# Optimization experiments

Hardware: AMD Instinct MI355X
Metric: run time of the kernel (lower is better)

## Reference

```python
import jax, jax.numpy as jnp
import numpy as np
import math

N_NODES = 20000
N_EDGES = 640000
N_BASIS = 10
NUM_NEIGHBORS = 32.0


def _fctp_scalar_attr(x0, x1, attr, W0, W1):
    """FullyConnectedTensorProduct(irreps_in, '0e' attr) == per-irrep linear
    scaled by the scalar attribute, with e3nn fan-in normalization.
    x0: [N, mul0] scalars, x1: [N, mul1, 3] vectors, attr: [N, 1]."""
    a = attr[:, :1]
    y0 = (x0 * a) @ W0 / jnp.sqrt(jnp.asarray(W0.shape[0], x0.dtype))
    y1 = jnp.einsum('nui,uv->nvi', x1 * a[:, :, None], W1) / jnp.sqrt(jnp.asarray(W1.shape[0], x1.dtype))
    return y0, y1


def setup_inputs() -> dict:
    key = jax.random.key(0)
    ks = jax.random.split(key, 13)
    node_input = jax.random.normal(ks[0], (N_NODES, 80), jnp.float32)
    node_attr = jnp.ones((N_NODES, 1), jnp.float32)
    edge_attr = jax.random.normal(ks[1], (N_EDGES, 4), jnp.float32)
    edge_scalars = jax.random.uniform(ks[2], (N_EDGES, N_BASIS), jnp.float32)
    edge_index = jax.random.randint(ks[3], (2, N_EDGES), 0, N_NODES)
    # learned params
    W_sc0 = jax.random.normal(ks[4], (32, 32), jnp.float32)
    W_sc1 = jax.random.normal(ks[5], (16, 16), jnp.float32)
    W_l1_0 = jax.random.normal(ks[6], (32, 32), jnp.float32)
    W_l1_1 = jax.random.normal(ks[7], (16, 16), jnp.float32)
    W_fc0 = jax.random.normal(ks[8], (N_BASIS, 64), jnp.float32)
    W_fc1 = jax.random.normal(ks[9], (64, 96), jnp.float32)  # 96 = tp.weight_numel
    W_l2_0 = jax.random.normal(ks[10], (48, 32), jnp.float32)
    W_l2_1 = jax.random.normal(ks[11], (48, 16), jnp.float32)
    return dict(node_input=node_input, node_attr=node_attr, edge_attr=edge_attr,
                edge_scalars=edge_scalars, W_sc0=W_sc0, W_sc1=W_sc1,
                W_l1_0=W_l1_0, W_l1_1=W_l1_1, W_fc0=W_fc0, W_fc1=W_fc1,
                W_l2_0=W_l2_0, W_l2_1=W_l2_1, edge_index=edge_index)


def reference(node_input, node_attr, edge_attr, edge_scalars,
              W_sc0, W_sc1, W_l1_0, W_l1_1, W_fc0, W_fc1, W_l2_0, W_l2_1,
              edge_index):
    N = node_input.shape[0]
    x0 = node_input[:, :32]                     # 32x0e
    x1 = node_input[:, 32:].reshape(N, 16, 3)   # 16x1o

    # self-connection and pre-TP linear
    s0, s1 = _fctp_scalar_attr(x0, x1, node_attr, W_sc0, W_sc1)
    y0, y1 = _fctp_scalar_attr(x0, x1, node_attr, W_l1_0, W_l1_1)

    # radial MLP -> per-edge TP weights (e3nn FullyConnectedNet: no bias, fan-in norm, silu)
    h = jax.nn.silu(edge_scalars @ W_fc0 / jnp.sqrt(jnp.asarray(N_BASIS, jnp.float32)))
    w = h @ W_fc1 / jnp.sqrt(jnp.asarray(64.0, jnp.float32))  # [E, 96]
    w_a, w_b, w_c, w_d = w[:, :32], w[:, 32:64], w[:, 64:80], w[:, 80:96]

    src, dst = edge_index[0], edge_index[1]
    xs0 = y0[src]                               # [E, 32]
    xs1 = y1[src]                               # [E, 16, 3]
    e0 = edge_attr[:, :1]                       # [E, 1] 0e sh
    e1 = edge_attr[:, 1:4]                      # [E, 3] 1o sh

    # 'uvu' tensor product paths -> irreps_mid = 32x0e + 16x0e + 32x1o + 16x1o
    m_a = w_a * xs0 * e0                                    # 0e x 0e -> 0e  [E,32]
    m_b = (w_b * xs0)[:, :, None] * e1[:, None, :]          # 0e x 1o -> 1o  [E,32,3]
    m_c = w_c[:, :, None] * xs1 * e0[:, :, None]            # 1o x 0e -> 1o  [E,16,3]
    m_d = w_d * jnp.einsum('eui,ei->eu', xs1, e1) / jnp.sqrt(jnp.asarray(3.0, jnp.float32))  # 1o x 1o -> 0e [E,16]
    mid0 = jnp.concatenate([m_a, m_d], axis=1)              # [E, 48] scalars
    mid1 = jnp.concatenate([m_b, m_c], axis=1)              # [E, 48, 3] vectors

    # scatter-add into destination nodes, normalized by sqrt(num_neighbors)
    inv = 1.0 / jnp.sqrt(jnp.asarray(NUM_NEIGHBORS, jnp.float32))
    agg0 = jax.ops.segment_sum(mid0, dst, num_segments=N) * inv
    agg1 = jax.ops.segment_sum(mid1, dst, num_segments=N) * inv

    # lin2: FCTP(irreps_mid, '0e') -> irreps_out, attr == 1
    z0 = agg0 @ W_l2_0 / jnp.sqrt(jnp.asarray(48.0, jnp.float32))
    z1 = jnp.einsum('nui,uv->nvi', agg1, W_l2_1) / jnp.sqrt(jnp.asarray(48.0, jnp.float32))

    # skip mix: output_mask of sc is all ones here (all out irreps reachable)
    c_s = math.sin(math.pi / 8)
    c_x = math.cos(math.pi / 8)
    out0 = c_s * s0 + c_x * z0
    out1 = c_s * s1 + c_x * z1
    return jnp.concatenate([out0, out1.reshape(N, 48)], axis=1)
```

## Files before the change

kernel.cpp:

```cpp
#include <hip/hip_runtime.h>

#define N_NODES 20000
#define N_EDGES 640000
#define N_MT (N_EDGES/16)

typedef short short8 __attribute__((ext_vector_type(8)));
typedef float f32x4 __attribute__((ext_vector_type(4)));

__device__ __forceinline__ unsigned short f2bf(float x){
  unsigned int u = __builtin_bit_cast(unsigned int, x);
  u += 0x7fffu + ((u >> 16) & 1u);
  return (unsigned short)(u >> 16);
}

__device__ __forceinline__ void wave_lds_fence(){
  __asm__ volatile("s_waitcnt lgkmcnt(0)" ::: "memory");
}

__global__ void k_y(const float* __restrict__ ni, const float* __restrict__ na,
                    const float* __restrict__ Wl10, const float* __restrict__ Wl11,
                    float* __restrict__ y){
  int gid = blockIdx.x*256 + threadIdx.x;
  if (gid >= N_NODES*80) return;
  int n = gid / 80, k = gid - n*80;
  const float* row = ni + (size_t)n*80;
  float a = na[n];
  float acc = 0.f;
  if (k < 32){
    #pragma unroll
    for (int u=0; u<32; ++u) acc += row[u]*Wl10[u*32+k];
    y[gid] = acc * a * 0.17677669529663687f;
  } else {
    int kk = k-32, v = kk/3, i = kk - v*3;
    #pragma unroll
    for (int u=0; u<16; ++u) acc += row[32+u*3+i]*Wl11[u*16+v];
    y[gid] = acc * a * 0.25f;
  }
}

__global__ void k_hist(const int* __restrict__ ei, int* __restrict__ counts){
  int e = blockIdx.x*256 + threadIdx.x;
  if (e < N_EDGES) atomicAdd(&counts[ei[N_EDGES + e]], 1);
}

__global__ void k_alloc(const int* __restrict__ counts, int* __restrict__ ctr,
                        int* __restrict__ cursor){
  int n = blockIdx.x*256 + threadIdx.x;
  if (n < N_NODES) cursor[n] = atomicAdd(ctr, counts[n]);
}

__global__ void k_fill(const int* __restrict__ ei, int* __restrict__ cursor,
                       int* __restrict__ eids, int* __restrict__ srcs,
                       int* __restrict__ dsts){
  int e = blockIdx.x*256 + threadIdx.x;
  if (e < N_EDGES){
    int d = ei[N_EDGES + e];
    int pos = atomicAdd(&cursor[d], 1);
    eids[pos] = e;
    srcs[pos] = ei[e];
    dsts[pos] = d;
  }
}

__global__ __launch_bounds__(256, 3) void k_edge(
    const float* __restrict__ edge_attr, const float* __restrict__ edge_scalars,
    const float* __restrict__ Wfc0, const float* __restrict__ Wfc1,
    const int* __restrict__ eids, const int* __restrict__ srcs,
    const int* __restrict__ dsts,
    const float* __restrict__ y, float* __restrict__ agg){
  __shared__ float s_wfc0[640];
  __shared__ float s_w [4][16*97];
  __shared__ float s_y [4][16*80];
  __shared__ float s_es[4][16*16];
  __shared__ float s_ea[4][16*4];

  const int t = threadIdx.x;
  const int w = t >> 6, l = t & 63;
  const int r = l & 15, part = l >> 4;

  for (int i = t; i < 640; i += 256) s_wfc0[i] = Wfc0[i];

  short8 b0[6], b1[6];
  #pragma unroll
  for (int nt=0; nt<6; ++nt){
    #pragma unroll
    for (int j=0; j<8; ++j){
      b0[nt][j] = (short)f2bf(Wfc1[(     part*8+j)*96 + nt*16 + r]);
      b1[nt][j] = (short)f2bf(Wfc1[(32 + part*8+j)*96 + nt*16 + r]);
    }
  }
  __syncthreads();

  int o_c[3], yo[3], eai[3];
  bool dot0;
  {
    #pragma unroll
    for (int p=0; p<3; ++p){
      int c = p*64 + l;
      if (c < 32)      { o_c[p]=c;    yo[p]=c;        eai[p]=0; }
      else if (c < 48) { int u=c-32;  o_c[p]=80+u;    yo[p]=32+3*u; eai[p]=0; }
      else if (c < 144){ int idx=c-48;  int u=idx/3, fi=idx-u*3; o_c[p]=32+u; yo[p]=u;        eai[p]=1+fi; }
      else             { int idx=c-144; int u=idx/3, i =idx-u*3; o_c[p]=64+u; yo[p]=32+3*u+i; eai[p]=0; }
    }
    dot0 = (l >= 32) && (l < 48);
  }

  float* sw  = s_w[w];
  float* sy  = s_y[w];
  float* ses = s_es[w];
  float* sea = s_ea[w];

  const int gw = blockIdx.x*4 + w;
  const int nw = gridDim.x*4;
  const int m0 = (int)(((long long)gw     * N_MT) / nw);
  const int m1 = (int)(((long long)(gw+1) * N_MT) / nw);

  float acc0 = 0.f, acc1 = 0.f, acc2 = 0.f;
  int dcur = -1;

  for (int m = m0; m < m1; ++m){
    const int base = m*16;
    const int eid  = eids[base + r];
    const int srcv = srcs[base + r];
    const int dstv = dsts[base + r];

    {
      const float* esp = edge_scalars + (size_t)eid*10;
      if (part == 0)      *(float4*)(ses + r*16    ) = *(const float4*)(esp);
      else if (part == 1) *(float4*)(ses + r*16 + 4) = *(const float4*)(esp + 4);
      else if (part == 2) *(float2*)(ses + r*16 + 8) = *(const float2*)(esp + 8);
      else                *(float4*)(sea + r*4     ) = *(const float4*)(edge_attr + (size_t)eid*4);
      const float* yp = y + (size_t)srcv*80 + part*20;
      float* syp = sy + r*80 + part*20;
      #pragma unroll
      for (int q=0; q<5; ++q)
        *(float4*)(syp + q*4) = *(const float4*)(yp + q*4);
    }
    wave_lds_fence();

    float hv0[8], hv1[8];
    #pragma unroll
    for (int j=0; j<8; ++j){ hv0[j]=0.f; hv1[j]=0.f; }
    {
      const float* esr = ses + r*16;
      #pragma unroll
      for (int k=0; k<10; ++k){
        float ev = esr[k];
        const float* wr = s_wfc0 + k*64 + part*8;
        #pragma unroll
        for (int j=0; j<8; ++j){ hv0[j] += ev*wr[j]; hv1[j] += ev*wr[32+j]; }
      }
    }
    short8 a0, a1;
    #pragma unroll
    for (int j=0; j<8; ++j){
      float x0 = hv0[j]*0.31622776601683794f;
      float x1 = hv1[j]*0.31622776601683794f;
      a0[j] = (short)f2bf(x0/(1.f+__expf(-x0)));
      a1[j] = (short)f2bf(x1/(1.f+__expf(-x1)));
    }

    #pragma unroll
    for (int nt=0; nt<6; ++nt){
      f32x4 acc = {0.f,0.f,0.f,0.f};
      acc = __builtin_amdgcn_mfma_f32_16x16x32_bf16(a0, b0[nt], acc, 0,0,0);
      acc = __builtin_amdgcn_mfma_f32_16x16x32_bf16(a1, b1[nt], acc, 0,0,0);
      #pragma unroll
      for (int rr=0; rr<4; ++rr)
        sw[(part*4+rr)*97 + nt*16 + r] = acc[rr]*0.125f;
    }
    wave_lds_fence();

    for (int e=0; e<16; ++e){
      int de = __shfl(dstv, e);
      if (de != dcur){
        if (dcur >= 0){
          unsafeAtomicAdd(&agg[(size_t)dcur*192 +       l], acc0);
          unsafeAtomicAdd(&agg[(size_t)dcur*192 +  64 + l], acc1);
          unsafeAtomicAdd(&agg[(size_t)dcur*192 + 128 + l], acc2);
        }
        acc0 = acc1 = acc2 = 0.f;
        dcur = de;
      }
      const float* swe  = sw  + e*97;
      const float* sye  = sy  + e*80;
      const float* seae = sea + e*4;
      float m0v;
      if (dot0){
        m0v = swe[o_c[0]] * (sye[yo[0]]*seae[1] + sye[yo[0]+1]*seae[2] + sye[yo[0]+2]*seae[3])
              * 0.5773502691896258f;
      } else {
        m0v = swe[o_c[0]] * sye[yo[0]] * seae[eai[0]];
      }
      acc0 += m0v;
      acc1 += swe[o_c[1]] * sye[yo[1]] * seae[eai[1]];
      acc2 += swe[o_c[2]] * sye[yo[2]] * seae[eai[2]];
    }
    wave_lds_fence();
  }
  if (dcur >= 0){
    unsafeAtomicAdd(&agg[(size_t)dcur*192 +       l], acc0);
    unsafeAtomicAdd(&agg[(size_t)dcur*192 +  64 + l], acc1);
    unsafeAtomicAdd(&agg[(size_t)dcur*192 + 128 + l], acc2);
  }
}

__global__ void k_finish(const float* __restrict__ ni, const float* __restrict__ na,
    const float* __restrict__ Wsc0, const float* __restrict__ Wsc1,
    const float* __restrict__ Wl20, const float* __restrict__ Wl21,
    const float* __restrict__ agg, float* __restrict__ out){
  int gid = blockIdx.x*256 + threadIdx.x;
  if (gid >= N_NODES*80) return;
  int n = gid / 80, k = gid - n*80;
  const float* row = ni + (size_t)n*80;
  const float* ag  = agg + (size_t)n*192;
  float a = na[n];
  const float c_s = 0.3826834323650898f;
  const float c_x = 0.9238795325112867f;
  const float zscale = 0.17677669529663687f * 0.14433756729740643f;
  float s = 0.f, z = 0.f;
  if (k < 32){
    #pragma unroll
    for (int u=0; u<32; ++u) s += row[u]*Wsc0[u*32+k];
    s *= a * 0.17677669529663687f;
    #pragma unroll
    for (int u=0; u<48; ++u) z += ag[u]*Wl20[u*32+k];
  } else {
    int kk=k-32, v=kk/3, i=kk-v*3;
    #pragma unroll
    for (int u=0; u<16; ++u) s += row[32+u*3+i]*Wsc1[u*16+v];
    s *= a * 0.25f;
    #pragma unroll
    for (int u=0; u<48; ++u) z += ag[48+u*3+i]*Wl21[u*16+v];
  }
  out[gid] = c_s*s + c_x*z*zscale;
}

extern "C" void kernel_launch(void* const* d_in, const int* in_sizes, int n_in,
                              void* d_out, int out_size, void* d_ws, size_t ws_size,
                              hipStream_t stream){
  const float* node_input   = (const float*)d_in[0];
  const float* node_attr    = (const float*)d_in[1];
  const float* edge_attr    = (const float*)d_in[2];
  const float* edge_scalars = (const float*)d_in[3];
  const float* W_sc0 = (const float*)d_in[4];
  const float* W_sc1 = (const float*)d_in[5];
  const float* W_l1_0 = (const float*)d_in[6];
  const float* W_l1_1 = (const float*)d_in[7];
  const float* W_fc0 = (const float*)d_in[8];
  const float* W_fc1 = (const float*)d_in[9];
  const float* W_l2_0 = (const float*)d_in[10];
  const float* W_l2_1 = (const float*)d_in[11];
  const int* edge_index = (const int*)d_in[12];
  float* out = (float*)d_out;

  char* ws = (char*)d_ws;
  float* y    = (float*)ws;
  float* agg  = (float*)(ws + 6400000);
  int* counts = (int*)(ws + 6400000 + 15360000);
  int* ctr    = counts + 20000;
  int* cursor = counts + 20008;
  int* eids   = cursor + 20000;
  int* srcs   = eids + N_EDGES;
  int* dsts   = srcs + N_EDGES;

  hipMemsetAsync(agg, 0, (size_t)N_NODES*192*sizeof(float), stream);
  hipMemsetAsync(counts, 0, (size_t)(20008)*sizeof(int), stream);

  k_hist <<<(N_EDGES+255)/256, 256, 0, stream>>>(edge_index, counts);
  k_alloc<<<(N_NODES+255)/256, 256, 0, stream>>>(counts, ctr, cursor);
  k_fill <<<(N_EDGES+255)/256, 256, 0, stream>>>(edge_index, cursor, eids, srcs, dsts);
  k_y    <<<(N_NODES*80+255)/256, 256, 0, stream>>>(node_input, node_attr, W_l1_0, W_l1_1, y);
  k_edge <<<768, 256, 0, stream>>>(edge_attr, edge_scalars, W_fc0, W_fc1,
                                   eids, srcs, dsts, y, agg);
  k_finish<<<(N_NODES*80+255)/256, 256, 0, stream>>>(node_input, node_attr, W_sc0, W_sc1,
                                                     W_l2_0, W_l2_1, agg, out);
}
```

Before: 381.7 us.

## Pack sorted edge metadata, prefetch next tile, fuse histogram with node linear

The fill kernel now writes a packed 64-byte record per sorted edge holding src, dst, edge_attr and edge_scalars, so the edge kernel reads one contiguous, coalesced float4 per lane instead of gathering through eids. The edge kernel software-pipelines the work: the next tile's metadata and source-node y rows are loaded into registers while the current tile's MLP and MFMA run. Edge scalars now reach lanes by shuffles rather than LDS, and the LDS row stride for the weights changes. The histogram and y kernels are merged into one launch. The cost is an extra 41MB scattered write in k_fill and higher register pressure from the prefetch buffers.

Measured after the change: 579.3 us. +51.8%, slower.

```diff
diff --git a/kernel.cpp b/kernel.cpp
--- a/kernel.cpp
+++ b/kernel.cpp
@@ -17,10 +17,19 @@
   __asm__ volatile("s_waitcnt lgkmcnt(0)" ::: "memory");
 }
 
-__global__ void k_y(const float* __restrict__ ni, const float* __restrict__ na,
-                    const float* __restrict__ Wl10, const float* __restrict__ Wl11,
-                    float* __restrict__ y){
-  int gid = blockIdx.x*256 + threadIdx.x;
+#define HIST_BLOCKS ((N_EDGES+255)/256)
+#define Y_BLOCKS    ((N_NODES*80+255)/256)
+
+__global__ void k_pre(const int* __restrict__ ei, int* __restrict__ counts,
+                      const float* __restrict__ ni, const float* __restrict__ na,
+                      const float* __restrict__ Wl10, const float* __restrict__ Wl11,
+                      float* __restrict__ y){
+  if (blockIdx.x < HIST_BLOCKS){
+    int e = blockIdx.x*256 + threadIdx.x;
+    if (e < N_EDGES) atomicAdd(&counts[ei[N_EDGES + e]], 1);
+    return;
+  }
+  int gid = (blockIdx.x - HIST_BLOCKS)*256 + threadIdx.x;
   if (gid >= N_NODES*80) return;
   int n = gid / 80, k = gid - n*80;
   const float* row = ni + (size_t)n*80;
@@ -38,41 +47,38 @@
   }
 }
 
-__global__ void k_hist(const int* __restrict__ ei, int* __restrict__ counts){
-  int e = blockIdx.x*256 + threadIdx.x;
-  if (e < N_EDGES) atomicAdd(&counts[ei[N_EDGES + e]], 1);
-}
-
 __global__ void k_alloc(const int* __restrict__ counts, int* __restrict__ ctr,
                         int* __restrict__ cursor){
   int n = blockIdx.x*256 + threadIdx.x;
   if (n < N_NODES) cursor[n] = atomicAdd(ctr, counts[n]);
 }
 
-__global__ void k_fill(const int* __restrict__ ei, int* __restrict__ cursor,
-                       int* __restrict__ eids, int* __restrict__ srcs,
-                       int* __restrict__ dsts){
+__global__ void k_fill(const int* __restrict__ ei, const float* __restrict__ ea,
+                       const float* __restrict__ es, int* __restrict__ cursor,
+                       float4* __restrict__ meta){
   int e = blockIdx.x*256 + threadIdx.x;
-  if (e < N_EDGES){
-    int d = ei[N_EDGES + e];
-    int pos = atomicAdd(&cursor[d], 1);
-    eids[pos] = e;
-    srcs[pos] = ei[e];
-    dsts[pos] = d;
-  }
+  if (e >= N_EDGES) return;
+  int s = ei[e], d = ei[N_EDGES + e];
+  int pos = atomicAdd(&cursor[d], 1);
+  const float* eap = ea + (size_t)e*4;
+  const float* esp = es + (size_t)e*10;
+  float4 v0, v1, v2, v3;
+  v0.x = __int_as_float(s); v0.y = __int_as_float(d); v0.z = eap[0]; v0.w = eap[1];
+  v1.x = eap[2]; v1.y = eap[3]; v1.z = esp[0]; v1.w = esp[1];
+  v2.x = esp[2]; v2.y = esp[3]; v2.z = esp[4]; v2.w = esp[5];
+  v3.x = esp[6]; v3.y = esp[7]; v3.z = esp[8]; v3.w = esp[9];
+  float4* mp = meta + (size_t)pos*4;
+  mp[0] = v0; mp[1] = v1; mp[2] = v2; mp[3] = v3;
 }
 
 __global__ __launch_bounds__(256, 3) void k_edge(
-    const float* __restrict__ edge_attr, const float* __restrict__ edge_scalars,
+    const float4* __restrict__ meta,
     const float* __restrict__ Wfc0, const float* __restrict__ Wfc1,
-    const int* __restrict__ eids, const int* __restrict__ srcs,
-    const int* __restrict__ dsts,
     const float* __restrict__ y, float* __restrict__ agg){
   __shared__ float s_wfc0[640];
-  __shared__ float s_w [4][16*97];
+  __shared__ float s_w [4][16*98];
   __shared__ float s_y [4][16*80];
-  __shared__ float s_es[4][16*16];
-  __shared__ float s_ea[4][16*4];
+  __shared__ float s_m [4][16*16];
 
   const int t = threadIdx.x;
   const int w = t >> 6, l = t & 63;
@@ -92,64 +98,65 @@
   __syncthreads();
 
   int o_c[3], yo[3], eai[3];
-  bool dot0;
-  {
-    #pragma unroll
-    for (int p=0; p<3; ++p){
-      int c = p*64 + l;
-      if (c < 32)      { o_c[p]=c;    yo[p]=c;        eai[p]=0; }
-      else if (c < 48) { int u=c-32;  o_c[p]=80+u;    yo[p]=32+3*u; eai[p]=0; }
-      else if (c < 144){ int idx=c-48;  int u=idx/3, fi=idx-u*3; o_c[p]=32+u; yo[p]=u;        eai[p]=1+fi; }
-      else             { int idx=c-144; int u=idx/3, i =idx-u*3; o_c[p]=64+u; yo[p]=32+3*u+i; eai[p]=0; }
-    }
-    dot0 = (l >= 32) && (l < 48);
-  }
-
-  float* sw  = s_w[w];
-  float* sy  = s_y[w];
-  float* ses = s_es[w];
-  float* sea = s_ea[w];
+  #pragma unroll
+  for (int p=0; p<3; ++p){
+    int c = p*64 + l;
+    if (c < 32)      { o_c[p]=c;    yo[p]=c;        eai[p]=0; }
+    else if (c < 48) { int u=c-32;  o_c[p]=80+u;    yo[p]=32+3*u; eai[p]=0; }
+    else if (c < 144){ int idx=c-48;  int u=idx/3, fi=idx-u*3; o_c[p]=32+u; yo[p]=u;        eai[p]=1+fi; }
+    else             { int idx=c-144; int u=idx/3, i =idx-u*3; o_c[p]=64+u; yo[p]=32+3*u+i; eai[p]=0; }
+  }
+  const bool dot0 = (l >= 32) && (l < 48);
+
+  float* sw = s_w[w];
+  float* sy = s_y[w];
+  float* sm = s_m[w];
 
   const int gw = blockIdx.x*4 + w;
   const int nw = gridDim.x*4;
   const int m0 = (int)(((long long)gw     * N_MT) / nw);
   const int m1 = (int)(((long long)(gw+1) * N_MT) / nw);
+  if (m0 >= m1) return;
+
+  float4 mreg = meta[(size_t)m0*64 + l];
+  float4 yreg[5];
+  {
+    int srcv = __float_as_int(__shfl(mreg.x, 4*r));
+    const float4* yp = (const float4*)(y + (size_t)srcv*80 + part*20);
+    #pragma unroll
+    for (int q=0; q<5; ++q) yreg[q] = yp[q];
+  }
 
   float acc0 = 0.f, acc1 = 0.f, acc2 = 0.f;
   int dcur = -1;
 
   for (int m = m0; m < m1; ++m){
-    const int base = m*16;
-    const int eid  = eids[base + r];
-    const int srcv = srcs[base + r];
-    const int dstv = dsts[base + r];
-
+    *(float4*)(sm + l*4) = mreg;
     {
-      const float* esp = edge_scalars + (size_t)eid*10;
-      if (part == 0)      *(float4*)(ses + r*16    ) = *(const float4*)(esp);
-      else if (part == 1) *(float4*)(ses + r*16 + 4) = *(const float4*)(esp + 4);
-      else if (part == 2) *(float2*)(ses + r*16 + 8) = *(const float2*)(esp + 8);
-      else                *(float4*)(sea + r*4     ) = *(const float4*)(edge_attr + (size_t)eid*4);
-      const float* yp = y + (size_t)srcv*80 + part*20;
-      float* syp = sy + r*80 + part*20;
-      #pragma unroll
-      for (int q=0; q<5; ++q)
-        *(float4*)(syp + q*4) = *(const float4*)(yp + q*4);
-    }
+      float4* syp = (float4*)(sy + r*80 + part*20);
+      #pragma unroll
+      for (int q=0; q<5; ++q) syp[q] = yreg[q];
+    }
+    const float4 mcur = mreg;
+    const bool have_next = (m+1 < m1);
+    if (have_next) mreg = meta[(size_t)(m+1)*64 + l];
     wave_lds_fence();
 
+    float esv[10];
+    esv[0]=__shfl(mcur.z, 4*r+1); esv[1]=__shfl(mcur.w, 4*r+1);
+    esv[2]=__shfl(mcur.x, 4*r+2); esv[3]=__shfl(mcur.y, 4*r+2);
+    esv[4]=__shfl(mcur.z, 4*r+2); esv[5]=__shfl(mcur.w, 4*r+2);
+    esv[6]=__shfl(mcur.x, 4*r+3); esv[7]=__shfl(mcur.y, 4*r+3);
+    esv[8]=__shfl(mcur.z, 4*r+3); esv[9]=__shfl(mcur.w, 4*r+3);
     float hv0[8], hv1[8];
     #pragma unroll
     for (int j=0; j<8; ++j){ hv0[j]=0.f; hv1[j]=0.f; }
-    {
-      const float* esr = ses + r*16;
-      #pragma unroll
-      for (int k=0; k<10; ++k){
-        float ev = esr[k];
-        const float* wr = s_wfc0 + k*64 + part*8;
-        #pragma unroll
-        for (int j=0; j<8; ++j){ hv0[j] += ev*wr[j]; hv1[j] += ev*wr[32+j]; }
-      }
+    #pragma unroll
+    for (int k=0; k<10; ++k){
+      float ev = esv[k];
+      const float* wr = s_wfc0 + k*64 + part*8;
+      #pragma unroll
+      for (int j=0; j<8; ++j){ hv0[j] += ev*wr[j]; hv1[j] += ev*wr[32+j]; }
     }
     short8 a0, a1;
     #pragma unroll
@@ -160,6 +167,13 @@
       a1[j] = (short)f2bf(x1/(1.f+__expf(-x1)));
     }
 
+    if (have_next){
+      int srcv = __float_as_int(__shfl(mreg.x, 4*r));
+      const float4* yp = (const float4*)(y + (size_t)srcv*80 + part*20);
+      #pragma unroll
+      for (int q=0; q<5; ++q) yreg[q] = yp[q];
+    }
+
     #pragma unroll
     for (int nt=0; nt<6; ++nt){
       f32x4 acc = {0.f,0.f,0.f,0.f};
@@ -167,12 +181,13 @@
       acc = __builtin_amdgcn_mfma_f32_16x16x32_bf16(a1, b1[nt], acc, 0,0,0);
       #pragma unroll
       for (int rr=0; rr<4; ++rr)
-        sw[(part*4+rr)*97 + nt*16 + r] = acc[rr]*0.125f;
+        sw[(part*4+rr)*98 + nt*16 + r] = acc[rr]*0.125f;
     }
     wave_lds_fence();
 
     for (int e=0; e<16; ++e){
-      int de = __shfl(dstv, e);
+      const float* sme = sm + e*16;
+      int de = __float_as_int(sme[1]);
       if (de != dcur){
         if (dcur >= 0){
           unsafeAtomicAdd(&agg[(size_t)dcur*192 +       l], acc0);
@@ -182,19 +197,18 @@
         acc0 = acc1 = acc2 = 0.f;
         dcur = de;
       }
-      const float* swe  = sw  + e*97;
-      const float* sye  = sy  + e*80;
-      const float* seae = sea + e*4;
+      const float* swe = sw + e*98;
+      const float* sye = sy + e*80;
       float m0v;
       if (dot0){
-        m0v = swe[o_c[0]] * (sye[yo[0]]*seae[1] + sye[yo[0]+1]*seae[2] + sye[yo[0]+2]*seae[3])
+        m0v = swe[o_c[0]] * (sye[yo[0]]*sme[3] + sye[yo[0]+1]*sme[4] + sye[yo[0]+2]*sme[5])
               * 0.5773502691896258f;
       } else {
-        m0v = swe[o_c[0]] * sye[yo[0]] * seae[eai[0]];
+        m0v = swe[o_c[0]] * sye[yo[0]] * sme[2 + eai[0]];
       }
       acc0 += m0v;
-      acc1 += swe[o_c[1]] * sye[yo[1]] * seae[eai[1]];
-      acc2 += swe[o_c[2]] * sye[yo[2]] * seae[eai[2]];
+      acc1 += swe[o_c[1]] * sye[yo[1]] * sme[2 + eai[1]];
+      acc2 += swe[o_c[2]] * sye[yo[2]] * sme[2 + eai[2]];
     }
     wave_lds_fence();
   }
@@ -255,24 +269,22 @@
   float* out = (float*)d_out;
 
   char* ws = (char*)d_ws;
-  float* y    = (float*)ws;
-  float* agg  = (float*)(ws + 6400000);
-  int* counts = (int*)(ws + 6400000 + 15360000);
-  int* ctr    = counts + 20000;
-  int* cursor = counts + 20008;
-  int* eids   = cursor + 20000;
-  int* srcs   = eids + N_EDGES;
-  int* dsts   = srcs + N_EDGES;
+  float*  y    = (float*)ws;
+  float*  agg  = (float*)(ws + 6400000);
+  float4* meta = (float4*)(ws + 21760000);
+  int* counts  = (int*)(ws + 62720000);
+  int* ctr     = counts + 20000;
+  int* cursor  = counts + 20008;
 
   hipMemsetAsync(agg, 0, (size_t)N_NODES*192*sizeof(float), stream);
-  hipMemsetAsync(counts, 0, (size_t)(20008)*sizeof(int), stream);
-
-  k_hist <<<(N_EDGES+255)/256, 256, 0, stream>>>(edge_index, counts);
+  hipMemsetAsync(counts, 0, (size_t)20008*sizeof(int), stream);
+
+  k_pre  <<<HIST_BLOCKS + Y_BLOCKS, 256, 0, stream>>>(edge_index, counts,
+                                                      node_input, node_attr, W_l1_0, W_l1_1, y);
   k_alloc<<<(N_NODES+255)/256, 256, 0, stream>>>(counts, ctr, cursor);
-  k_fill <<<(N_EDGES+255)/256, 256, 0, stream>>>(edge_index, cursor, eids, srcs, dsts);
-  k_y    <<<(N_NODES*80+255)/256, 256, 0, stream>>>(node_input, node_attr, W_l1_0, W_l1_1, y);
-  k_edge <<<768, 256, 0, stream>>>(edge_attr, edge_scalars, W_fc0, W_fc1,
-                                   eids, srcs, dsts, y, agg);
+  k_fill <<<(N_EDGES+255)/256, 256, 0, stream>>>(edge_index, edge_attr, edge_scalars,
+                                                 cursor, meta);
+  k_edge <<<768, 256, 0, stream>>>(meta, W_fc0, W_fc1, y, agg);
   k_finish<<<(N_NODES*80+255)/256, 256, 0, stream>>>(node_input, node_attr, W_sc0, W_sc1,
                                                      W_l2_0, W_l2_1, agg, out);
 }
```
